# Optimization experiments

Hardware: AMD Instinct MI355X
Metric: run time of the kernel (lower is better)

## Reference

```python
import jax, jax.numpy as jnp
import numpy as np

B, T, D, H, NL = 64, 1024, 64, 256, 2


def setup_inputs() -> dict:
    key = jax.random.key(0)
    ks = jax.random.split(key, 12)
    s_ih0 = 1.0 / np.sqrt(H)
    inp = {
        "x": jax.random.normal(ks[0], (B, T, D), dtype=jnp.float32),
        "W_ih0": jax.random.uniform(ks[1], (4 * H, D), jnp.float32, -s_ih0, s_ih0),
        "W_hh0": jax.random.uniform(ks[2], (4 * H, H), jnp.float32, -s_ih0, s_ih0),
        "b_ih0": jax.random.uniform(ks[3], (4 * H,), jnp.float32, -s_ih0, s_ih0),
        "b_hh0": jax.random.uniform(ks[4], (4 * H,), jnp.float32, -s_ih0, s_ih0),
        "W_ih1": jax.random.uniform(ks[5], (4 * H, H), jnp.float32, -s_ih0, s_ih0),
        "W_hh1": jax.random.uniform(ks[6], (4 * H, H), jnp.float32, -s_ih0, s_ih0),
        "b_ih1": jax.random.uniform(ks[7], (4 * H,), jnp.float32, -s_ih0, s_ih0),
        "b_hh1": jax.random.uniform(ks[8], (4 * H,), jnp.float32, -s_ih0, s_ih0),
        "fc_w": jax.random.uniform(ks[9], (1, H), jnp.float32, -s_ih0, s_ih0),
        "fc_b": jax.random.uniform(ks[10], (1,), jnp.float32, -s_ih0, s_ih0),
    }
    return inp


def _lstm_layer(x, W_ih, W_hh, b_ih, b_hh):
    # x: [B, T, Din] -> hidden sequence [B, T, H]
    h = W_hh.shape[1]
    # precompute input contribution for all timesteps (PyTorch gate order i,f,g,o)
    xg = jnp.einsum('btd,gd->btg', x, W_ih) + b_ih + b_hh  # [B, T, 4H]

    def step(carry, xt):
        hprev, cprev = carry
        gates = xt + hprev @ W_hh.T  # [B, 4H]
        i, f, g, o = jnp.split(gates, 4, axis=-1)
        i = jax.nn.sigmoid(i)
        f = jax.nn.sigmoid(f)
        g = jnp.tanh(g)
        o = jax.nn.sigmoid(o)
        c = f * cprev + i * g
        hnew = o * jnp.tanh(c)
        return (hnew, c), hnew

    b = x.shape[0]
    h0 = jnp.zeros((b, h), x.dtype)
    _, hs = jax.lax.scan(step, (h0, h0), jnp.swapaxes(xg, 0, 1))
    return jnp.swapaxes(hs, 0, 1)  # [B, T, H]


def reference(x, W_ih0, W_hh0, b_ih0, b_hh0, W_ih1, W_hh1, b_ih1, b_hh1, fc_w, fc_b):
    h1 = _lstm_layer(x, W_ih0, W_hh0, b_ih0, b_hh0)
    h2 = _lstm_layer(h1, W_ih1, W_hh1, b_ih1, b_hh1)
    last = h2[:, -1, :]  # [B, H]
    return last @ fc_w.T + fc_b  # [B, 1]
```

## Files before the change

kernel.cpp:

```cpp
#include <hip/hip_runtime.h>

#define B_ 64
#define TT 1024
#define HH 256

__device__ __forceinline__ float sigmoidf_(float x) { return 1.f / (1.f + __expf(-x)); }
__device__ __forceinline__ float fast_tanh(float x) {
    float e = __expf(2.f * x);
    return 1.f - 2.f / (e + 1.f);
}

__global__ __launch_bounds__(256) void xgemm_kernel(
    const float* __restrict__ A, const float* __restrict__ W,
    const float* __restrict__ bih, const float* __restrict__ bhh,
    float* __restrict__ out,
    int K, int RINGA, int s0A, int LC, int astr)
{
    __shared__ float As[16][132];
    __shared__ float Bs[16][132];
    const int tid = threadIdx.x;
    const int bm = (int)blockIdx.x >> 3;
    const int bn = (int)blockIdx.x & 7;
    const int m0 = bm << 7, n0 = bn << 7;
    const int ty = tid >> 4, tx = tid & 15;
    const int CM = (1 << LC) - 1;

    const float* arow[8];
    const float* brow[8];
#pragma unroll
    for (int i = 0; i < 8; ++i) {
        int mm = m0 + i * 16 + ty;
        int bb = mm >> LC, tc = mm & CM;
        int slot = s0A + tc; if (slot >= RINGA) slot -= RINGA;
        arow[i] = A + ((size_t)bb * RINGA + slot) * K * astr + tx * astr;
        brow[i] = W + (size_t)(n0 + i * 16 + ty) * K + tx;
    }

    float acc[8][8];
#pragma unroll
    for (int i = 0; i < 8; ++i)
#pragma unroll
        for (int j = 0; j < 8; ++j) acc[i][j] = 0.f;

    for (int kc = 0; kc < K; kc += 16) {
#pragma unroll
        for (int i = 0; i < 8; ++i) {
            As[tx][i * 16 + ty] = arow[i][kc * astr];
            Bs[tx][i * 16 + ty] = brow[i][kc];
        }
        __syncthreads();
#pragma unroll
        for (int k = 0; k < 16; ++k) {
            float a[8], bf[8];
#pragma unroll
            for (int j = 0; j < 8; ++j) a[j] = As[k][ty * 8 + j];
#pragma unroll
            for (int j = 0; j < 8; ++j) bf[j] = Bs[k][tx * 8 + j];
#pragma unroll
            for (int i = 0; i < 8; ++i)
#pragma unroll
                for (int j = 0; j < 8; ++j) acc[i][j] = fmaf(a[i], bf[j], acc[i][j]);
        }
        __syncthreads();
    }

    float bias[8];
#pragma unroll
    for (int j = 0; j < 8; ++j) bias[j] = bih[n0 + tx * 8 + j] + bhh[n0 + tx * 8 + j];
#pragma unroll
    for (int i = 0; i < 8; ++i) {
        float4 v0 = make_float4(acc[i][0] + bias[0], acc[i][1] + bias[1],
                                acc[i][2] + bias[2], acc[i][3] + bias[3]);
        float4 v1 = make_float4(acc[i][4] + bias[4], acc[i][5] + bias[5],
                                acc[i][6] + bias[6], acc[i][7] + bias[7]);
        size_t o = (size_t)(m0 + ty * 8 + i) * 1024 + n0 + tx * 8;
        *(float4*)&out[o] = v0;
        *(float4*)&out[o + 4] = v1;
    }
}

__global__ __launch_bounds__(1024)
__attribute__((amdgpu_waves_per_eu(4, 4)))
void recur_chunk(
    const float* __restrict__ xg,
    const float* __restrict__ Whh,
    unsigned long long* __restrict__ hring,
    float* __restrict__ cstate,
    int t0, int nsteps, int s0, int RING, int LC, int first)
{
    const int tid = threadIdx.x;
    const int b = (int)blockIdx.x & 63;
    const int q = (int)blockIdx.x >> 6;
    const int w = tid >> 6;
    const int l = tid & 63;
    const int r = tid >> 2;
    const int c4 = tid & 3;
    const int gr = ((r >> 6) << 8) + (q << 6) + (r & 63);

    __shared__ __align__(16) float sh_h[272];
    __shared__ float sh_gate[256];

    float4 w4[16];
    {
        const float4* src = (const float4*)(Whh + (size_t)gr * 256 + (c4 << 6));
#pragma unroll
        for (int j = 0; j < 16; ++j) w4[j] = src[j];
    }
#pragma unroll
    for (int j = 0; j < 16; ++j)
        asm volatile("" : "+v"(w4[j].x), "+v"(w4[j].y), "+v"(w4[j].z), "+v"(w4[j].w));

    const size_t hbB = (size_t)b * RING;
    float c = 0.f;
    if (!first && tid < 64) c = cstate[((int)blockIdx.x << 6) + tid];
    if (tid < 272) sh_h[tid] = 0.f;
    if (!first && tid < 256) {
        int sprev = (s0 == 0) ? RING - 1 : s0 - 1;
        unsigned long long v = hring[(hbB + sprev) * 256 + tid];
        sh_h[tid + ((tid >> 6) << 2)] = __uint_as_float((unsigned)v);
    }
    __syncthreads();

    const float4* h4 = (const float4*)(sh_h + c4 * 68);

    for (int tc = 0; tc < nsteps; ++tc) {
        const int t = t0 + tc;
        int slot = s0 + tc; if (slot >= RING) slot -= RING;
        const size_t srow = (hbB + slot) * 256;

        float xgv = 0.f;
        if (c4 == 0) xgv = xg[((size_t)((b << LC) + tc) << 10) + gr];

        float acc = 0.f;
#pragma unroll
        for (int j = 0; j < 16; ++j) {
            float4 hv = h4[j], wv = w4[j];
            acc = fmaf(wv.x, hv.x, acc);
            acc = fmaf(wv.y, hv.y, acc);
            acc = fmaf(wv.z, hv.z, acc);
            acc = fmaf(wv.w, hv.w, acc);
        }
        acc += __shfl_xor(acc, 1);
        acc += __shfl_xor(acc, 2);
        if (c4 == 0) sh_gate[r] = acc + xgv;
        __syncthreads();

        if (w == 0) {
            float gi = sh_gate[l];
            float gf = sh_gate[64 + l];
            float gg = sh_gate[128 + l];
            float go = sh_gate[192 + l];
            float i_ = sigmoidf_(gi);
            float f_ = sigmoidf_(gf);
            float g_ = fast_tanh(gg);
            float o_ = sigmoidf_(go);
            c = fmaf(f_, c, i_ * g_);
            float hn = o_ * fast_tanh(c);
            sh_h[q * 68 + l] = hn;
            unsigned long long word =
                ((unsigned long long)(unsigned)t << 32) | __float_as_uint(hn);
            __hip_atomic_store(&hring[srow + (q << 6) + l], word,
                               __ATOMIC_RELAXED, __HIP_MEMORY_SCOPE_AGENT);
        } else if (w <= 3) {
            const int p = (q + w) & 3;
            unsigned long long* src = &hring[srow + (p << 6) + l];
            unsigned long long v;
            for (;;) {
                v = __hip_atomic_load(src, __ATOMIC_RELAXED,
                                      __HIP_MEMORY_SCOPE_AGENT);
                if ((int)(v >> 32) == t) break;
                __builtin_amdgcn_s_sleep(1);
            }
            sh_h[p * 68 + l] = __uint_as_float((unsigned)v);
        }
        __syncthreads();
    }

    if (tid < 64) cstate[((int)blockIdx.x << 6) + tid] = c;
}

__global__ void fc_kernel(const unsigned long long* __restrict__ h2r,
                          int slot_last, int RING,
                          const float* __restrict__ fcw, const float* __restrict__ fcb,
                          float* __restrict__ out)
{
    int b = threadIdx.x;
    if (b < 64) {
        const unsigned long long* h = h2r + ((size_t)b * RING + slot_last) * 256;
        float acc = 0.f;
        for (int d = 0; d < HH; ++d)
            acc = fmaf(__uint_as_float((unsigned)h[d]), fcw[d], acc);
        out[b] = acc + fcb[0];
    }
}

extern "C" void kernel_launch(void* const* d_in, const int* in_sizes, int n_in,
                              void* d_out, int out_size, void* d_ws, size_t ws_size,
                              hipStream_t stream)
{
    const float* x     = (const float*)d_in[0];
    const float* W_ih0 = (const float*)d_in[1];
    const float* W_hh0 = (const float*)d_in[2];
    const float* b_ih0 = (const float*)d_in[3];
    const float* b_hh0 = (const float*)d_in[4];
    const float* W_ih1 = (const float*)d_in[5];
    const float* W_hh1 = (const float*)d_in[6];
    const float* b_ih1 = (const float*)d_in[7];
    const float* b_hh1 = (const float*)d_in[8];
    const float* fc_w  = (const float*)d_in[9];
    const float* fc_b  = (const float*)d_in[10];
    float* out = (float*)d_out;

    auto need = [](size_t CH) -> size_t {
        return 4ull * (65536ull * CH
                     + 65536ull * (CH + 1)
                     + 32768ull);
    };
    int CHUNK = 32, LC = 5;
    if      (ws_size >= need(256)) { CHUNK = 256; LC = 8; }
    else if (ws_size >= need(128)) { CHUNK = 128; LC = 7; }
    else if (ws_size >= need(64))  { CHUNK = 64;  LC = 6; }
    const int RING = CHUNK + 1;

    float* ws  = (float*)d_ws;
    float* xgc = ws;
    unsigned long long* h1r =
        (unsigned long long*)(xgc + 65536ull * CHUNK);
    unsigned long long* h2r = h1r + 16384ull * RING;
    float* c0 = (float*)(h2r + 16384ull * RING);
    float* c1 = c0 + 16384;

    const int nchunks = TT / CHUNK;
    const int gemmblk = (B_ * CHUNK / 128) * 8;

    for (int k = 0; k < nchunks; ++k) {
        const int t0 = k * CHUNK;
        const int s0 = t0 % RING;
        const int first = (k == 0) ? 1 : 0;

        xgemm_kernel<<<dim3(gemmblk), dim3(256), 0, stream>>>(
            x, W_ih0, b_ih0, b_hh0, xgc, 64, TT, t0, LC, 1);
        recur_chunk<<<dim3(256), dim3(1024), 0, stream>>>(
            xgc, W_hh0, h1r, c0, t0, CHUNK, s0, RING, LC, first);

        xgemm_kernel<<<dim3(gemmblk), dim3(256), 0, stream>>>(
            (const float*)h1r, W_ih1, b_ih1, b_hh1, xgc, 256, RING, s0, LC, 2);
        recur_chunk<<<dim3(256), dim3(1024), 0, stream>>>(
            xgc, W_hh1, h2r, c1, t0, CHUNK, s0, RING, LC, first);
    }

    const int slot_last = (TT - 1) % RING;
    fc_kernel<<<dim3(1), dim3(64), 0, stream>>>(h2r, slot_last, RING, fc_w, fc_b, out);
}
```

Baseline: 3.572 ms.

## Halve recurrent block size, give each thread 128 weights, prefetch next xg

The recurrent kernel now runs 512 threads per block instead of 1024. Each thread holds 128 W_hh weights in registers (two halves of a row, split by lane half) instead of 64, so only one cross-lane shuffle is needed in place of two. The input-gate value for the next step is prefetched one iteration ahead, and sched_barriers split the dot product into stages. In exchange, register pressure doubles and per-thread serial FMA work grows, which may lengthen each timestep's latency.

```diff
diff --git a/kernel.cpp b/kernel.cpp
--- a/kernel.cpp
+++ b/kernel.cpp
@@ -79,8 +79,8 @@
     }
 }
 
-__global__ __launch_bounds__(1024)
-__attribute__((amdgpu_waves_per_eu(4, 4)))
+__global__ __launch_bounds__(512)
+__attribute__((amdgpu_waves_per_eu(2, 2)))
 void recur_chunk(
     const float* __restrict__ xg,
     const float* __restrict__ Whh,
@@ -93,21 +93,30 @@
     const int q = (int)blockIdx.x >> 6;
     const int w = tid >> 6;
     const int l = tid & 63;
-    const int r = tid >> 2;
-    const int c4 = tid & 3;
+    const int hf = l >> 5;
+    const int r = (w << 5) + (l & 31);
     const int gr = ((r >> 6) << 8) + (q << 6) + (r & 63);
 
     __shared__ __align__(16) float sh_h[272];
     __shared__ float sh_gate[256];
 
-    float4 w4[16];
+    float4 w4[32];
     {
-        const float4* src = (const float4*)(Whh + (size_t)gr * 256 + (c4 << 6));
-#pragma unroll
-        for (int j = 0; j < 16; ++j) w4[j] = src[j];
-    }
-#pragma unroll
-    for (int j = 0; j < 16; ++j)
+        const float4* src = (const float4*)(Whh + (size_t)gr * 256 + (hf << 7));
+#pragma unroll
+        for (int j = 0; j < 32; ++j) w4[j] = src[j];
+    }
+#pragma unroll
+    for (int j = 0; j < 8; ++j)
+        asm volatile("" : "+v"(w4[j].x), "+v"(w4[j].y), "+v"(w4[j].z), "+v"(w4[j].w));
+#pragma unroll
+    for (int j = 8; j < 16; ++j)
+        asm volatile("" : "+v"(w4[j].x), "+v"(w4[j].y), "+v"(w4[j].z), "+v"(w4[j].w));
+#pragma unroll
+    for (int j = 16; j < 24; ++j)
+        asm volatile("" : "+v"(w4[j].x), "+v"(w4[j].y), "+v"(w4[j].z), "+v"(w4[j].w));
+#pragma unroll
+    for (int j = 24; j < 32; ++j)
         asm volatile("" : "+v"(w4[j].x), "+v"(w4[j].y), "+v"(w4[j].z), "+v"(w4[j].w));
 
     const size_t hbB = (size_t)b * RING;
@@ -121,28 +130,53 @@
     }
     __syncthreads();
 
-    const float4* h4 = (const float4*)(sh_h + c4 * 68);
+    const float4* h4a = (const float4*)(sh_h + hf * 136);
+    const float4* h4b = (const float4*)(sh_h + hf * 136 + 68);
+    const float* xgp = xg + ((size_t)(b << LC) << 10) + gr;
+
+    float xgv = (hf == 0) ? xgp[0] : 0.f;
 
     for (int tc = 0; tc < nsteps; ++tc) {
         const int t = t0 + tc;
         int slot = s0 + tc; if (slot >= RING) slot -= RING;
         const size_t srow = (hbB + slot) * 256;
 
-        float xgv = 0.f;
-        if (c4 == 0) xgv = xg[((size_t)((b << LC) + tc) << 10) + gr];
+        float xgn = 0.f;
+        if (hf == 0 && tc + 1 < nsteps) xgn = xgp[(size_t)(tc + 1) << 10];
 
         float acc = 0.f;
 #pragma unroll
-        for (int j = 0; j < 16; ++j) {
-            float4 hv = h4[j], wv = w4[j];
-            acc = fmaf(wv.x, hv.x, acc);
-            acc = fmaf(wv.y, hv.y, acc);
-            acc = fmaf(wv.z, hv.z, acc);
-            acc = fmaf(wv.w, hv.w, acc);
-        }
-        acc += __shfl_xor(acc, 1);
-        acc += __shfl_xor(acc, 2);
-        if (c4 == 0) sh_gate[r] = acc + xgv;
+        for (int j = 0; j < 8; ++j) {
+            float4 hv = h4a[j], wv = w4[j];
+            acc = fmaf(wv.x, hv.x, acc); acc = fmaf(wv.y, hv.y, acc);
+            acc = fmaf(wv.z, hv.z, acc); acc = fmaf(wv.w, hv.w, acc);
+        }
+        __builtin_amdgcn_sched_barrier(0);
+#pragma unroll
+        for (int j = 8; j < 16; ++j) {
+            float4 hv = h4a[j], wv = w4[j];
+            acc = fmaf(wv.x, hv.x, acc); acc = fmaf(wv.y, hv.y, acc);
+            acc = fmaf(wv.z, hv.z, acc); acc = fmaf(wv.w, hv.w, acc);
+        }
+        __builtin_amdgcn_sched_barrier(0);
+#pragma unroll
+        for (int j = 0; j < 8; ++j) {
+            float4 hv = h4b[j], wv = w4[16 + j];
+            acc = fmaf(wv.x, hv.x, acc); acc = fmaf(wv.y, hv.y, acc);
+            acc = fmaf(wv.z, hv.z, acc); acc = fmaf(wv.w, hv.w, acc);
+        }
+        __builtin_amdgcn_sched_barrier(0);
+#pragma unroll
+        for (int j = 8; j < 16; ++j) {
+            float4 hv = h4b[j], wv = w4[16 + j];
+            acc = fmaf(wv.x, hv.x, acc); acc = fmaf(wv.y, hv.y, acc);
+            acc = fmaf(wv.z, hv.z, acc); acc = fmaf(wv.w, hv.w, acc);
+        }
+        __builtin_amdgcn_sched_barrier(0);
+
+        acc += __shfl_xor(acc, 32);
+        if (hf == 0) sh_gate[r] = acc + xgv;
+        xgv = xgn;
         __syncthreads();
 
         if (w == 0) {
@@ -240,12 +274,12 @@
 
         xgemm_kernel<<<dim3(gemmblk), dim3(256), 0, stream>>>(
             x, W_ih0, b_ih0, b_hh0, xgc, 64, TT, t0, LC, 1);
-        recur_chunk<<<dim3(256), dim3(1024), 0, stream>>>(
+        recur_chunk<<<dim3(256), dim3(512), 0, stream>>>(
             xgc, W_hh0, h1r, c0, t0, CHUNK, s0, RING, LC, first);
 
         xgemm_kernel<<<dim3(gemmblk), dim3(256), 0, stream>>>(
             (const float*)h1r, W_ih1, b_ih1, b_hh1, xgc, 256, RING, s0, LC, 2);
-        recur_chunk<<<dim3(256), dim3(1024), 0, stream>>>(
+        recur_chunk<<<dim3(256), dim3(512), 0, stream>>>(
             xgc, W_hh1, h2r, c1, t0, CHUNK, s0, RING, LC, first);
     }
 
```

New measurement: 3.699 ms. 1.04x slower.
